# Kernel tuning notes

Measured on AMD Instinct MI355X. Metric: run time of the kernel, lower is better.

Reference implementation:

```python
import math
import numpy as np
import jax, jax.numpy as jnp

C = 8  # hidden multiplicity (num_channels)
B, N = 4, 4096

# ---------- real Wigner 3j (e3nn convention: Frobenius norm 1) ----------

def _su2_cg(l1, l2, l3):
    f = math.factorial
    def cg(m1, m2, m3):
        if m1 + m2 != m3:
            return 0.0
        pref = math.sqrt((2 * l3 + 1) * f(l3 + l1 - l2) * f(l3 - l1 + l2) * f(l1 + l2 - l3) / f(l1 + l2 + l3 + 1))
        pref *= math.sqrt(f(l3 + m3) * f(l3 - m3) * f(l1 - m1) * f(l1 + m1) * f(l2 - m2) * f(l2 + m2))
        s = 0.0
        for k in range(l1 + l2 - l3 + 1):
            d = [k, l1 + l2 - l3 - k, l1 - m1 - k, l2 + m2 - k, l3 - l2 + m1 + k, l3 - l1 - m2 + k]
            if min(d) < 0:
                continue
            s += (-1.0) ** k / np.prod([float(f(x)) for x in d])
        return pref * s
    out = np.zeros((2 * l1 + 1, 2 * l2 + 1, 2 * l3 + 1))
    for i, m1 in enumerate(range(-l1, l1 + 1)):
        for j, m2 in enumerate(range(-l2, l2 + 1)):
            for k, m3 in enumerate(range(-l3, l3 + 1)):
                out[i, j, k] = cg(m1, m2, m3)
    return out

def _q_real_to_complex(l):
    q = np.zeros((2 * l + 1, 2 * l + 1), dtype=np.complex128)
    rs2 = 1.0 / math.sqrt(2.0)
    for m in range(-l, 0):
        q[l + m, l + abs(m)] = rs2
        q[l + m, l - abs(m)] = -1j * rs2
    q[l, l] = 1.0
    for m in range(1, l + 1):
        q[l + m, l + abs(m)] = (-1) ** m * rs2
        q[l + m, l - abs(m)] = 1j * (-1) ** m * rs2
    return (-1j) ** l * q

def _w3j(l1, l2, l3):
    Q1, Q2, Q3 = _q_real_to_complex(l1), _q_real_to_complex(l2), _q_real_to_complex(l3)
    Cc = _su2_cg(l1, l2, l3).astype(np.complex128)
    Cr = np.real(np.einsum('ij,kl,mn,ikm->jln', Q1, Q2, np.conj(Q3), Cc))
    return (Cr / np.linalg.norm(Cr)).astype(np.float32)

# tensor-product paths (selection rules for 4e/6e inputs, 0e/2e SH, 4e/6e outputs)
VAL_PATHS = [(4, 0, 4), (4, 2, 4), (6, 2, 4), (4, 2, 6), (6, 0, 6), (6, 2, 6)]
OUT_PATHS = [(4, 4, 4), (4, 6, 4), (6, 4, 4), (6, 6, 4), (4, 4, 6), (4, 6, 6), (6, 4, 6), (6, 6, 6)]
# path normalization ('element'): fan-in = 3*C for tp_val outputs, 4*C^2 for tp_out outputs
W3J_VAL = [jnp.asarray(_w3j(*p) * math.sqrt((2 * p[2] + 1) / (3.0 * C))) for p in VAL_PATHS]
W3J_OUT = [jnp.asarray(_w3j(*p) * math.sqrt((2 * p[2] + 1) / (4.0 * C * C))) for p in OUT_PATHS]


def _forward(feat, sh_lr, log_s, pos_w, pos_b, w_lin_in, w_val, w_out, w_lin_out):
    b, n, _ = feat.shape
    f4, f6 = feat[..., :9], feat[..., 9:]                      # 1x4e, 1x6e
    f4n = f4 / jnp.maximum(jnp.linalg.norm(f4, axis=-1, keepdims=True), 1e-12)
    f6n = f6 / jnp.maximum(jnp.linalg.norm(f6, axis=-1, keepdims=True), 1e-12)
    s4, s6 = jnp.exp(log_s[0]), jnp.exp(log_s[1])
    scores = s4 * jnp.einsum('bnd,bmd->bnm', f4n, f4n) + s6 * jnp.einsum('bnd,bmd->bnm', f6n, f6n)
    pb = sh_lr @ pos_w + pos_b                                 # (N,)
    scores = scores + (pb[:, None] + pb[None, :])[None]
    attn = jax.nn.softmax(scores.astype(jnp.float32), axis=-1).astype(feat.dtype)

    h4 = f4[:, :, None, :] * w_lin_in[0][None, None, :, None]  # (B,N,C,9)
    h6 = f6[:, :, None, :] * w_lin_in[1][None, None, :, None]  # (B,N,C,13)

    y = {0: sh_lr[:, :1], 2: sh_lr[:, 1:]}                     # (N,1), (N,5)
    hx = {4: h4, 6: h6}
    v = {4: jnp.zeros((b, n, C, 9), feat.dtype), 6: jnp.zeros((b, n, C, 13), feat.dtype)}
    for p, (l1, l2, l3) in enumerate(VAL_PATHS):
        v[l3] = v[l3] + jnp.einsum('bnui,nj,ijk,uw->bnwk', hx[l1], y[l2], W3J_VAL[p], w_val[p])
    vals = jnp.concatenate([v[4].reshape(b, n, 9 * C), v[6].reshape(b, n, 13 * C)], axis=-1)

    ctx = jnp.einsum('bnm,bmd->bnd', attn, vals)               # (B,N,22C)
    cx = {4: ctx[..., :9 * C].reshape(b, n, C, 9), 6: ctx[..., 9 * C:].reshape(b, n, C, 13)}
    o = {4: jnp.zeros((b, n, C, 9), feat.dtype), 6: jnp.zeros((b, n, C, 13), feat.dtype)}
    for p, (l1, l2, l3) in enumerate(OUT_PATHS):
        o[l3] = o[l3] + jnp.einsum('bnui,bnvj,ijk,uvw->bnwk', hx[l1], cx[l2], W3J_OUT[p], w_out[p])

    inv_sc = 1.0 / math.sqrt(C)                                # lin_out fan_in = C
    d4 = jnp.einsum('bnui,u->bni', o[4], w_lin_out[0]) * inv_sc
    d6 = jnp.einsum('bnui,u->bni', o[6], w_lin_out[1]) * inv_sc
    return jnp.concatenate([d4, d6], axis=-1)                  # (B,N,22)


def setup_inputs() -> dict:
    key = jax.random.key(0)
    ks = jax.random.split(key, 8)
    feat = jax.random.normal(ks[0], (B, N, 22), jnp.float32)
    sh_lr = jax.random.normal(ks[1], (N, 6), jnp.float32)
    log_s = jnp.array([math.log(1.0 / 3.0), math.log(1.0 / math.sqrt(13.0))], jnp.float32)
    pos_w = 0.01 * jax.random.normal(ks[2], (6,), jnp.float32)
    pos_b = jnp.zeros((), jnp.float32)
    w_lin_in = jax.random.normal(ks[3], (2, C), jnp.float32)
    w_val = jax.random.normal(ks[4], (6, C, C), jnp.float32)
    w_out = jax.random.normal(ks[5], (8, C, C, C), jnp.float32)
    w_lin_out = jax.random.normal(ks[6], (2, C), jnp.float32)
    return dict(feat=feat, sh_lr=sh_lr, log_s=log_s, pos_w=pos_w, pos_b=pos_b,
                w_lin_in=w_lin_in, w_val=w_val, w_out=w_out, w_lin_out=w_lin_out)


def reference(feat, sh_lr, log_s, pos_w, pos_b, w_lin_in, w_val, w_out, w_lin_out):
    return _forward(feat, sh_lr, log_s, pos_w, pos_b, w_lin_in, w_val, w_out, w_lin_out)
```

## Files before the change

kernel.cpp:

```cpp
#include <hip/hip_runtime.h>
#include <cmath>

#define NN 4096
#define BB 4
#define CCH 8

#define OFF_W3JVAL 0
#define OFF_W3JOUT 2688
#define OFF_CTX0   13568
#define CTXS       1572864
#define OFFB_KGH   25220096ULL
#define OFFB_KGL   26268672ULL
#define OFFB_VG    27317248ULL
#define OFFB_WBH   30462976ULL
#define OFFB_WBL   30493696ULL

typedef short s16x8 __attribute__((ext_vector_type(8)));
typedef _Float16 f16x8 __attribute__((ext_vector_type(8)));
typedef float f32x4 __attribute__((ext_vector_type(4)));
typedef unsigned int u32x4 __attribute__((ext_vector_type(4)));
typedef unsigned int u32x2 __attribute__((ext_vector_type(2)));

static __device__ __forceinline__ unsigned short f2bf(float x){
  unsigned u = __float_as_uint(x);
  return (unsigned short)((u + 0x7FFFu + ((u >> 16) & 1u)) >> 16);
}
static __device__ __forceinline__ float bf2f(unsigned short h){
  return __uint_as_float(((unsigned)h) << 16);
}
static __device__ __forceinline__ unsigned pk2r(float v){
  unsigned short h = f2bf(v);
  unsigned short l = f2bf(v - bf2f(h));
  return ((unsigned)l << 16) | (unsigned)h;
}
static __device__ __forceinline__ unsigned short f2h(float x){
  return __builtin_bit_cast(unsigned short, (_Float16)x);
}
static __device__ __forceinline__ void unpk(u32x4 a, u32x4 b, s16x8& h, s16x8& l){
  u32x4 hw = { __builtin_amdgcn_perm(a[1],a[0],0x05040100u),
               __builtin_amdgcn_perm(a[3],a[2],0x05040100u),
               __builtin_amdgcn_perm(b[1],b[0],0x05040100u),
               __builtin_amdgcn_perm(b[3],b[2],0x05040100u)};
  u32x4 lw = { __builtin_amdgcn_perm(a[1],a[0],0x07060302u),
               __builtin_amdgcn_perm(a[3],a[2],0x07060302u),
               __builtin_amdgcn_perm(b[1],b[0],0x07060302u),
               __builtin_amdgcn_perm(b[3],b[2],0x07060302u)};
  h = __builtin_bit_cast(s16x8, hw);
  l = __builtin_bit_cast(s16x8, lw);
}

static __device__ __forceinline__ void qentf(int l, int r, int c, float& re, float& im){
  re=0.f; im=0.f;
  float s = ((l&3)==2)? -1.f : 1.f;
  const float rs2 = 0.70710678118654752440f;
  if(r < l){
    if(c == 2*l - r) re = s*rs2;
    else if(c == r)  im = -s*rs2;
  } else if(r == l){
    if(c == l) re = s;
  } else {
    float sg = ((r-l)&1)? -1.f : 1.f;
    if(c == r) re = s*sg*rs2;
    else if(c == 2*l - r) im = s*sg*rs2;
  }
}
__global__ __launch_bounds__(512) void k_tab(float* __restrict__ Wv, float* __restrict__ Wo){
  __shared__ float Ccf[2197];
  __shared__ float red[512];
  __shared__ double factS[20];
  int t = threadIdx.x;
  int p = blockIdx.x;
  if(t==0){
    double f=1.0; factS[0]=1.0;
    for(int i=1;i<20;i++){ f*=(double)i; factS[i]=f; }
  }
  const int L1[14]={4,4,6,4,6,6, 4,4,6,6,4,4,6,6};
  const int L2[14]={0,2,2,2,0,2, 4,6,4,6,4,6,4,6};
  const int L3[14]={4,4,4,6,6,6, 4,4,4,4,6,6,6,6};
  const int OFF[14]={0,81,486,1071,1656,1825, 0,729,1782,2835,4356,5409,6930,8451};
  int l1=L1[p], l2=L2[p], l3=L3[p];
  int d1=2*l1+1, d2=2*l2+1, d3=2*l3+1;
  int tot = d1*d2*d3;
  float* dst = (p<6) ? (Wv+OFF[p]) : (Wo+OFF[p]);
  float scale = (p<6) ? sqrtf((2.f*l3+1.f)/24.f) : sqrtf((2.f*l3+1.f)/256.f);
  __syncthreads();
  #pragma unroll 1
  for(int e=t; e<tot; e+=512){
    int i = e/(d2*d3), rem = e - i*(d2*d3), j = rem/d3, k = rem - j*d3;
    int m1=i-l1, m2=j-l2, m3=k-l3;
    double v=0.0;
    if(m1+m2==m3){
      double pref = sqrt((2.0*l3+1.0)*factS[l3+l1-l2]*factS[l3-l1+l2]*factS[l1+l2-l3]/factS[l1+l2+l3+1]);
      pref *= sqrt(factS[l3+m3]*factS[l3-m3]*factS[l1-m1]*factS[l1+m1]*factS[l2-m2]*factS[l2+m2]);
      double s=0.0;
      #pragma unroll 1
      for(int kk=0; kk<=l1+l2-l3; kk++){
        int dd0=kk, dd1=l1+l2-l3-kk, dd2=l1-m1-kk, dd3=l2+m2-kk, dd4=l3-l2+m1+kk, dd5=l3-l1-m2+kk;
        int mn=dd0;
        if(dd1<mn)mn=dd1; if(dd2<mn)mn=dd2; if(dd3<mn)mn=dd3; if(dd4<mn)mn=dd4; if(dd5<mn)mn=dd5;
        if(mn<0) continue;
        double prod = factS[dd0]*factS[dd1]*factS[dd2]*factS[dd3]*factS[dd4]*factS[dd5];
        s += ((kk&1)? -1.0:1.0)/prod;
      }
      v = pref*s;
    }
    Ccf[e]=(float)v;
  }
  __syncthreads();
  float nacc=0.f;
  #pragma unroll 1
  for(int e=t; e<tot; e+=512){
    int j = e/(d2*d3), rem = e - j*(d2*d3), l = rem/d3, n = rem - l*d3;
    float re = 0.f;
    #pragma unroll
    for(int ii=0; ii<2; ii++){
      int i = ii ? (2*l1 - j) : j;
      float q1r,q1i; qentf(l1,i,j,q1r,q1i);
      if(ii && i==j){ q1r=0.f; q1i=0.f; }
      #pragma unroll
      for(int kk=0; kk<2; kk++){
        int k = kk ? (2*l2 - l) : l;
        float q2r,q2i; qentf(l2,k,l,q2r,q2i);
        if(kk && k==l){ q2r=0.f; q2i=0.f; }
        float ar = q1r*q2r - q1i*q2i;
        float ai = q1r*q2i + q1i*q2r;
        #pragma unroll
        for(int mm=0; mm<2; mm++){
          int m = mm ? (2*l3 - n) : n;
          float q3r,q3i; qentf(l3,m,n,q3r,q3i);
          if(mm && m==n){ q3r=0.f; q3i=0.f; }
          float coef = ar*q3r + ai*q3i;
          re = fmaf(coef, Ccf[(i*d2+k)*d3+m], re);
        }
      }
    }
    dst[e]=re;
    nacc = fmaf(re,re,nacc);
  }
  red[t]=nacc;
  __syncthreads();
  #pragma unroll 1
  for(int s=256;s>0;s>>=1){
    if(t<s) red[t]+=red[t+s];
    __syncthreads();
  }
  float c = scale/sqrtf(red[0]);
  #pragma unroll 1
  for(int e=t; e<tot; e+=512) dst[e]*=c;
}

__global__ void k_weights(const float* __restrict__ wli, const float* __restrict__ wval,
                          const float* __restrict__ wout, const float* __restrict__ wlo,
                          const float* __restrict__ Wv,
                          unsigned short* __restrict__ WBH, unsigned short* __restrict__ WBL){
  __shared__ float bws[48];
  __shared__ float scs[64];
  __shared__ float As[24];
  int t = threadIdx.x;
  if(t<48){
    const int val_l1[6]={0,0,1,0,1,1};
    int p=t>>3, w=t&7;
    float s=0.f;
    for(int u=0;u<8;u++) s = fmaf(wli[val_l1[p]*8+u], wval[(p*8+u)*8+w], s);
    bws[t]=s;
  }
  {
    const int out_l1[8]={0,0,1,1,0,0,1,1};
    const int out_l3[8]={0,0,0,0,1,1,1,1};
    int p=t>>3, v=t&7;
    float s=0.f;
    for(int u=0;u<8;u++){
      float a=wli[out_l1[p]*8+u];
      for(int w=0;w<8;w++) s = fmaf(wout[((p*8+u)*8+v)*8+w]*a, wlo[out_l3[p]*8+w], s);
    }
    scs[t]=s*0.35355339059327373f;
  }
  __syncthreads();
  if(t<24){
    int p=t/3, i3=t-3*p;
    int vp = (p&1)*3 + i3;
    float s=0.f;
    for(int w=0;w<8;w++) s = fmaf(scs[p*8+w], bws[vp*8+w], s);
    As[t]=s;
  }
  __syncthreads();
  int base = blockIdx.x*960;
  for(int k=0;k<15;k++){
    int cell = base + k*64 + t;
    int f = cell/160, c = cell - f*160;
    float v = 0.f;
    if(f < 88 && c < 132){
      int seg = f/22, off = f - seg*22;
      int even = (off < 9);
      int p = 2*seg + (even?0:1);
      int jo = even ? off : off-9;
      int l1, i, jj;
      if(c < 54){ l1=4; i=c/6; jj=c-6*i; }
      else { int cc=c-54; l1=6; i=cc/6; jj=cc-6*i; }
      if(even){
        if(l1==4 && jj==0)      v = As[p*3+0]*Wv[i*9+jo];
        else if(l1==4)          v = As[p*3+1]*Wv[81+(i*5+jj-1)*9+jo];
        else if(jj>=1)          v = As[p*3+2]*Wv[486+(i*5+jj-1)*9+jo];
      } else {
        if(l1==4 && jj>=1)      v = As[p*3+0]*Wv[1071+(i*5+jj-1)*13+jo];
        else if(l1==6 && jj==0) v = As[p*3+1]*Wv[1656+i*13+jo];
        else if(l1==6)          v = As[p*3+2]*Wv[1825+(i*5+jj-1)*13+jo];
      }
    } else if(f==88 && c==132){
      v = 1.0f;
    }
    unsigned short h = f2bf(v);
    WBH[cell] = h;
    WBL[cell] = f2bf(v - bf2f(h));
  }
}

__launch_bounds__(128)
__global__ void k_prep(const float* __restrict__ feat, const float* __restrict__ sh,
                       const float* __restrict__ log_s, const float* __restrict__ pos_w,
                       const float* __restrict__ pos_b,
                       const unsigned short* __restrict__ WBH,
                       const unsigned short* __restrict__ WBL,
                       unsigned short* __restrict__ Kgh, unsigned short* __restrict__ Kgl,
                       unsigned short* __restrict__ Vg){
  __shared__ __align__(16) unsigned int Pbuf[16*164];
  __shared__ unsigned int Po[96*17];
  __shared__ float epbs[16];
  int tid = threadIdx.x;
  int w2 = tid >> 6, lane = tid & 63;
  int lm = lane & 15, quad = lane >> 4;
  int seg = w2*4 + quad;
  int panel = blockIdx.x >> 2, mt = blockIdx.x & 3;
  int idxp = panel*64 + mt*16 + lm;
  int n = idxp & (NN-1);
  const float* fp = feat + (size_t)idxp*22;
  const float* shp = sh + n*6;
  float f[22];
  #pragma unroll
  for(int c=0;c<22;c++) f[c]=fp[c];
  float y[6];
  #pragma unroll
  for(int j=0;j<6;j++) y[j]=shp[j];
  if(tid<16){
    float pb = pos_b[0];
    #pragma unroll
    for(int j=0;j<6;j++) pb = fmaf(y[j], pos_w[j], pb);
    epbs[lm] = __expf(pb);
    float n4=0.f, n6=0.f;
    #pragma unroll
    for(int c=0;c<9;c++) n4 += f[c]*f[c];
    #pragma unroll
    for(int c=9;c<22;c++) n6 += f[c]*f[c];
    n4 = fmaxf(sqrtf(n4), 1e-12f);
    n6 = fmaxf(sqrtf(n6), 1e-12f);
    float s4 = __expf(log_s[0]), s6 = __expf(log_s[1]);
    float a4 = sqrtf(s4)/n4, a6 = sqrtf(s6)/n6;
    unsigned short* kph = Kgh + (size_t)idxp*32;
    unsigned short* kpl = Kgl + (size_t)idxp*32;
    #pragma unroll
    for(int c=0;c<22;c++){
      float qv = f[c] * (c<9 ? a4 : a6);
      unsigned short h = f2bf(qv);
      kph[c]=h; kpl[c]=f2bf(qv - bf2f(h));
    }
    #pragma unroll
    for(int c=22;c<32;c++){ kph[c]=0; kpl[c]=0; }
  }
  #pragma unroll
  for(int j4=0;j4<5;j4++){
    u32x4 wv;
    #pragma unroll
    for(int e=0;e<4;e++){
      int c = seg*20 + j4*4 + e;
      float pv;
      if(c<54){ int i=c/6, jj=c-6*i; pv = f[i]*y[jj]; }
      else if(c<132){ int cc=c-54; int i=cc/6, jj=cc-6*i; pv = f[9+i]*y[jj]; }
      else if(c==132) pv = 1.0f;
      else pv = 0.0f;
      wv[e] = pk2r(pv);
    }
    *(u32x4*)&Pbuf[lm*164 + seg*20 + j4*4] = wv;
  }
  __syncthreads();
  f32x4 acc[3];
  #pragma unroll
  for(int ft=0;ft<3;ft++)
    #pragma unroll
    for(int i=0;i<4;i++) acc[ft][i]=0.f;
  for(int kc=0;kc<5;kc++){
    const u32x4* ap = (const u32x4*)&Pbuf[lm*164 + kc*32 + quad*8];
    s16x8 Ah, Al;
    unpk(ap[0], ap[1], Ah, Al);
    #pragma unroll
    for(int ft=0;ft<3;ft++){
      int ftg = w2*3 + ft;
      size_t bo = (size_t)(ftg*16+lm)*160 + kc*32 + quad*8;
      s16x8 Bh = *(const s16x8*)(WBH + bo);
      s16x8 Bl = *(const s16x8*)(WBL + bo);
      f32x4 a = acc[ft];
      a = __builtin_amdgcn_mfma_f32_16x16x32_bf16(Al, Bl, a, 0,0,0);
      a = __builtin_amdgcn_mfma_f32_16x16x32_bf16(Al, Bh, a, 0,0,0);
      a = __builtin_amdgcn_mfma_f32_16x16x32_bf16(Ah, Bl, a, 0,0,0);
      a = __builtin_amdgcn_mfma_f32_16x16x32_bf16(Ah, Bh, a, 0,0,0);
      acc[ft] = a;
    }
  }
  #pragma unroll
  for(int r=0;r<4;r++){
    float e = epbs[quad*4 + r];
    #pragma unroll
    for(int ft=0;ft<3;ft++){
      int ftg = w2*3 + ft;
      Po[(ftg*16+lm)*17 + quad*4 + r] = (unsigned)f2h(acc[ft][r]*e);
    }
  }
  __syncthreads();
  unsigned int* vO32 = (unsigned int*)(Vg + (size_t)panel*96*64);
  #pragma unroll
  for(int wv=0; wv<6; wv++){
    int idx2 = wv*128 + tid;
    int g = idx2 >> 3, j = idx2 & 7;
    unsigned lo = Po[g*17 + 2*j] & 0xFFFFu;
    unsigned hi = Po[g*17 + 2*j + 1] & 0xFFFFu;
    vO32[g*32 + mt*8 + j] = lo | (hi<<16);
  }
}

#define LDSK  0
#define LDSKL 4096
#define LDSV  8192
#define BUFB  20480
__global__ __launch_bounds__(512)
__attribute__((amdgpu_waves_per_eu(2, 2)))
void k_attn(const unsigned short* __restrict__ Kgh,
            const unsigned short* __restrict__ Kgl,
            const unsigned short* __restrict__ Vg,
            float* __restrict__ ctx0){
  __shared__ __align__(16) unsigned char lds[2*BUFB];
  int tid = threadIdx.x;
  int lane = tid & 63, w = tid >> 6;
  int lm = lane & 15, quad = lane >> 4;
  int blk = blockIdx.x;
  int b = blk & 3, kh = (blk>>2)&3, qb = blk >> 4;
  const unsigned short* KhB = Kgh + (size_t)b*NN*32;
  const unsigned short* KlB = Kgl + (size_t)b*NN*32;
  const unsigned short* VB  = Vg  + (size_t)b*64*96*64;
  float* ctx = ctx0 + (size_t)kh*CTXS + (size_t)b*NN*96;

  s16x8 qh[2], ql[2];
  #pragma unroll
  for(int q2=0;q2<2;q2++){
    size_t ro = (size_t)(qb*256 + w*32 + q2*16 + lm)*32 + (size_t)quad*8;
    qh[q2] = *(const s16x8*)(KhB + ro);
    ql[q2] = *(const s16x8*)(KlB + ro);
  }

  int kro = lm*64 + ((quad ^ ((lm>>1)&3))<<4);
  int vr0 = lm*128 + (((0*4+quad) ^ (lm&7))<<4);
  int vr1 = lm*128 + (((1*4+quad) ^ (lm&7))<<4);

  int dofs[3], sofs[3], sreg[3];
  #pragma unroll
  for(int rep=0;rep<3;rep++){
    int g = tid + 512*rep;
    if(g < 512){
      int gk = g & 255;
      int row = gk>>2, col = gk&3;
      int t = row>>4, rr = row&15;
      int kact = 32*(t&1) + 8*(rr>>2) + 4*(t>>1) + (rr&3);
      sreg[rep] = (g<256)? 0 : 1;
      sofs[rep] = kact*64 + col*16;
      dofs[rep] = ((g<256)? LDSK : LDSKL) + row*64 + ((col ^ ((row>>1)&3))<<4);
    }
    else if(g < 1280){ int gv=g-512; sreg[rep]=2; sofs[rep]=gv*16;
      dofs[rep] = LDSV + (gv>>3)*128 + (((gv&7) ^ ((gv>>3)&7))<<4); }
    else { sreg[rep]=-1; sofs[rep]=0; dofs[rep]=0; }
  }

  f32x4 acc[2][6];
  #pragma unroll
  for(int q2=0;q2<2;q2++)
    #pragma unroll
    for(int ft=0;ft<6;ft++)
      #pragma unroll
      for(int i=0;i<4;i++) acc[q2][ft][i]=0.f;

  u32x4 stg0, stg1, stg2;

#define MFB(A,Bv,C) __builtin_amdgcn_mfma_f32_16x16x32_bf16(A,Bv,C,0,0,0)
#define MFH(A,Bv,C) __builtin_amdgcn_mfma_f32_16x16x32_f16(A,Bv,C,0,0,0)

#define STG_ISSUE(T) { \
  const char* kb_ = (const char*)(KhB + (size_t)(kh*16+(T))*2048); \
  const char* lb_ = (const char*)(KlB + (size_t)(kh*16+(T))*2048); \
  const char* vb_ = (const char*)(VB  + (size_t)(kh*16+(T))*6144); \
  { const char* sp_ = (sreg[0]==0)? kb_ : (sreg[0]==1)? lb_ : vb_; \
    stg0 = *(const u32x4*)(sp_ + sofs[0]); } \
  { const char* sp_ = (sreg[1]==0)? kb_ : (sreg[1]==1)? lb_ : vb_; \
    stg1 = *(const u32x4*)(sp_ + sofs[1]); } \
  if(sreg[2]>=0){ stg2 = *(const u32x4*)(vb_ + sofs[2]); } }

#define STG_WRITE(BN) { \
  *(u32x4*)&lds[(BN)*BUFB + dofs[0]] = stg0; \
  *(u32x4*)&lds[(BN)*BUFB + dofs[1]] = stg1; \
  if(sreg[2]>=0){ *(u32x4*)&lds[(BN)*BUFB + dofs[2]] = stg2; } }

#define COMPUTE(B) { \
  unsigned Wt[2][4][2]; \
  _Pragma("unroll") \
  for(int kt=0;kt<4;kt++){ \
    s16x8 kfh = *(const s16x8*)&lds[(B)*BUFB + LDSK  + kt*1024 + kro]; \
    s16x8 kfl = *(const s16x8*)&lds[(B)*BUFB + LDSKL + kt*1024 + kro]; \
    _Pragma("unroll") \
    for(int q2=0;q2<2;q2++){ \
      f32x4 s_ = {0.f,0.f,0.f,0.f}; \
      s_ = MFB(kfl, qh[q2], s_); \
      s_ = MFB(kfh, ql[q2], s_); \
      s_ = MFB(kfh, qh[q2], s_); \
      Wt[q2][kt][0] = (unsigned)f2h(__expf(s_[0])) | ((unsigned)f2h(__expf(s_[1]))<<16); \
      Wt[q2][kt][1] = (unsigned)f2h(__expf(s_[2])) | ((unsigned)f2h(__expf(s_[3]))<<16); \
    } \
  } \
  _Pragma("unroll") \
  for(int c=0;c<2;c++){ \
    u32x4 paw0 = {Wt[0][c][0], Wt[0][c][1], Wt[0][c+2][0], Wt[0][c+2][1]}; \
    u32x4 paw1 = {Wt[1][c][0], Wt[1][c][1], Wt[1][c+2][0], Wt[1][c+2][1]}; \
    f16x8 PA0 = __builtin_bit_cast(f16x8, paw0); \
    f16x8 PA1 = __builtin_bit_cast(f16x8, paw1); \
    int vro_ = c ? vr1 : vr0; \
    _Pragma("unroll") \
    for(int ft=0;ft<6;ft++){ \
      f16x8 vf = *(const f16x8*)&lds[(B)*BUFB + LDSV + ft*2048 + vro_]; \
      acc[0][ft] = MFH(PA0, vf, acc[0][ft]); \
      acc[1][ft] = MFH(PA1, vf, acc[1][ft]); } \
  } }

  STG_ISSUE(0);
  STG_WRITE(0);
  __syncthreads();

  #pragma unroll 1
  for(int tp=0; tp<8; tp++){
    int t0 = 2*tp;
    STG_ISSUE(t0+1);
    COMPUTE(0);
    STG_WRITE(1);
    __syncthreads();
    if(t0+2 < 16){ STG_ISSUE(t0+2); }
    COMPUTE(1);
    if(t0+2 < 16){ STG_WRITE(0); }
    __syncthreads();
  }

#undef MFB
#undef MFH
#undef STG_ISSUE
#undef STG_WRITE
#undef COMPUTE

  #pragma unroll
  for(int q2=0;q2<2;q2++){
    #pragma unroll
    for(int ft=0;ft<6;ft++){
      int col = ft*16 + lm;
      #pragma unroll
      for(int r=0;r<4;r++){
        int row = qb*256 + w*32 + q2*16 + quad*4 + r;
        ctx[(size_t)row*96 + col] = acc[q2][ft][r];
      }
    }
  }
}

__launch_bounds__(256, 4)
__global__ void k_out(const float* __restrict__ feat, const float* __restrict__ ctxA,
                      const float* __restrict__ w3jout, float* __restrict__ out){
  __shared__ float gbuf[16*45];
  __shared__ float fbuf[16*24];
  __shared__ float dls[4*64*13];
  __shared__ float inv[16];
  int tid = threadIdx.x;
  int typ = blockIdx.x & 1;
  int n0 = (blockIdx.x>>1)*16;
  int gc0 = typ*44;
  for(int i=tid;i<16*44;i+=256){
    int pt=i/44, c=i-pt*44;
    const float* base = ctxA + (size_t)(n0+pt)*96 + gc0 + c;
    gbuf[pt*45+c] = base[0]+base[CTXS]+base[2*CTXS]+base[3*CTXS];
  }
  for(int i=tid;i<16*22;i+=256){
    int pt=i/22, c=i-pt*22;
    fbuf[pt*24+c] = feat[(size_t)(n0+pt)*22+c];
  }
  if(tid<16){
    const float* bd = ctxA + (size_t)(n0+tid)*96 + 88;
    inv[tid] = 1.0f/(bd[0]+bd[CTXS]+bd[2*CTXS]+bd[3*CTXS]);
  }
  __syncthreads();
  int lane = tid&63, w = tid>>6;
  int pt = lane&15, sub = lane>>4;
  float fR[13], gR[13], d[13];
  {
    int FB = (w&2)?9:0;
    int fn = (w&2)?13:9;
    #pragma unroll 13
    for(int i=0;i<13;i++) fR[i] = (i<fn) ? fbuf[pt*24 + FB + i] : 0.f;
    int GBl = (w==0)?0:(w==1)?9:(w==2)?22:31;
    int jn = (w&1)?13:9;
    #pragma unroll 13
    for(int j=0;j<13;j++) gR[j] = (j<jn) ? gbuf[pt*45 + GBl + j] : 0.f;
  }
  #pragma unroll 13
  for(int k=0;k<13;k++) d[k]=0.f;

#define PATHR(ID,JD,KD,WO) \
  _Pragma("unroll") \
  for(int ii=0;ii<((ID)+3)/4;ii++){ int i=sub+4*ii; if(i<(ID)){ float fv=fR[i]; \
    _Pragma("unroll") \
    for(int j=0;j<(JD);j++){ float val=fv*gR[j]; \
      const float* wp = w3jout + (WO) + (i*(JD)+j)*(KD); \
      _Pragma("unroll") \
      for(int k=0;k<(KD);k++) d[k] = fmaf(val, wp[k], d[k]); } } }

  int pcase = typ*4 + w;
  switch(pcase){
    case 0: PATHR(9,9,9, 0)       break;
    case 1: PATHR(9,13,9, 729)    break;
    case 2: PATHR(13,9,9, 1782)   break;
    case 3: PATHR(13,13,9, 2835)  break;
    case 4: PATHR(9,9,13, 4356)   break;
    case 5: PATHR(9,13,13, 5409)  break;
    case 6: PATHR(13,9,13, 6930)  break;
    default:PATHR(13,13,13, 8451) break;
  }
#undef PATHR
  {
    float* dp = &dls[(w*64+lane)*13];
    #pragma unroll 13
    for(int k=0;k<13;k++) dp[k]=d[k];
  }
  __syncthreads();
  {
    int KD = typ?13:9;
    int kb = typ?9:0;
    int pt2 = tid&15, kc = tid>>4;
    if(kc < KD){
      float s = 0.f;
      #pragma unroll
      for(int ww=0;ww<4;ww++)
        #pragma unroll
        for(int ss=0;ss<4;ss++)
          s += dls[(ww*64 + ss*16 + pt2)*13 + kc];
      out[(size_t)(n0+pt2)*22 + kb + kc] = s*inv[pt2];
    }
  }
}

extern "C" void kernel_launch(void* const* d_in, const int* in_sizes, int n_in,
                              void* d_out, int out_size, void* d_ws, size_t ws_size,
                              hipStream_t stream){
  (void)in_sizes; (void)n_in; (void)out_size; (void)ws_size;
  const float* feat =(const float*)d_in[0];
  const float* sh   =(const float*)d_in[1];
  const float* log_s=(const float*)d_in[2];
  const float* pos_w=(const float*)d_in[3];
  const float* pos_b=(const float*)d_in[4];
  const float* wli  =(const float*)d_in[5];
  const float* wval =(const float*)d_in[6];
  const float* wout =(const float*)d_in[7];
  const float* wlo  =(const float*)d_in[8];
  float* outp=(float*)d_out;
  float* wsf=(float*)d_ws;

  unsigned short* Kgh=(unsigned short*)((char*)d_ws + OFFB_KGH);
  unsigned short* Kgl=(unsigned short*)((char*)d_ws + OFFB_KGL);
  unsigned short* Vg =(unsigned short*)((char*)d_ws + OFFB_VG);
  unsigned short* WBH=(unsigned short*)((char*)d_ws + OFFB_WBH);
  unsigned short* WBL=(unsigned short*)((char*)d_ws + OFFB_WBL);

  hipLaunchKernelGGL(k_tab, dim3(14), dim3(512), 0, stream,
                     wsf+OFF_W3JVAL, wsf+OFF_W3JOUT);
  hipLaunchKernelGGL(k_weights, dim3(16), dim3(64), 0, stream,
                     wli, wval, wout, wlo, wsf+OFF_W3JVAL, WBH, WBL);
  hipLaunchKernelGGL(k_prep, dim3(1024), dim3(128), 0, stream,
                     feat, sh, log_s, pos_w, pos_b, WBH, WBL,
                     Kgh, Kgl, Vg);
  hipLaunchKernelGGL(k_attn, dim3(256), dim3(512), 0, stream,
                     Kgh, Kgl, Vg, wsf+OFF_CTX0);
  hipLaunchKernelGGL(k_out, dim3(2048), dim3(256), 0, stream,
                     feat, wsf+OFF_CTX0, wsf+OFF_W3JOUT, outp);
}
```

Measured before the change: 176.8 us.

## Software-pipeline attention: overlap next tile's scores/exp with current tile's PV MFMAs

Splits the per-tile attention compute into a score/exp stage (SPH) and a P·V stage (PVH). The P·V for one key tile now runs alongside the score MFMAs and exp for the next tile, using a three-buffer LDS ring and register-held exp weights. The goal is to hide the dependency chain from score MFMA to exp to f16 pack to PV MFMA, and to give the scheduler independent MFMA and VALU work to interleave. The cost is 1.5x LDS use and extra live registers for the buffered weights, which could cause spills under the fixed 2-waves-per-EU bound.

```diff
diff --git a/kernel.cpp b/kernel.cpp
--- a/kernel.cpp
+++ b/kernel.cpp
@@ -336,7 +336,7 @@
             const unsigned short* __restrict__ Kgl,
             const unsigned short* __restrict__ Vg,
             float* __restrict__ ctx0){
-  __shared__ __align__(16) unsigned char lds[2*BUFB];
+  __shared__ __align__(16) unsigned char lds[3*BUFB];
   int tid = threadIdx.x;
   int lane = tid & 63, w = tid >> 6;
   int lm = lane & 15, quad = lane >> 4;
@@ -385,6 +385,7 @@
       #pragma unroll
       for(int i=0;i<4;i++) acc[q2][ft][i]=0.f;
 
+  unsigned Wt[3][2][4][2];
   u32x4 stg0, stg1, stg2;
 
 #define MFB(A,Bv,C) __builtin_amdgcn_mfma_f32_16x16x32_bf16(A,Bv,C,0,0,0)
@@ -405,8 +406,7 @@
   *(u32x4*)&lds[(BN)*BUFB + dofs[1]] = stg1; \
   if(sreg[2]>=0){ *(u32x4*)&lds[(BN)*BUFB + dofs[2]] = stg2; } }
 
-#define COMPUTE(B) { \
-  unsigned Wt[2][4][2]; \
+#define SPH(B,WB) { \
   _Pragma("unroll") \
   for(int kt=0;kt<4;kt++){ \
     s16x8 kfh = *(const s16x8*)&lds[(B)*BUFB + LDSK  + kt*1024 + kro]; \
@@ -417,14 +417,16 @@
       s_ = MFB(kfl, qh[q2], s_); \
       s_ = MFB(kfh, ql[q2], s_); \
       s_ = MFB(kfh, qh[q2], s_); \
-      Wt[q2][kt][0] = (unsigned)f2h(__expf(s_[0])) | ((unsigned)f2h(__expf(s_[1]))<<16); \
-      Wt[q2][kt][1] = (unsigned)f2h(__expf(s_[2])) | ((unsigned)f2h(__expf(s_[3]))<<16); \
+      Wt[WB][q2][kt][0] = (unsigned)f2h(__expf(s_[0])) | ((unsigned)f2h(__expf(s_[1]))<<16); \
+      Wt[WB][q2][kt][1] = (unsigned)f2h(__expf(s_[2])) | ((unsigned)f2h(__expf(s_[3]))<<16); \
     } \
-  } \
+  } }
+
+#define PVH(B,WB) { \
   _Pragma("unroll") \
   for(int c=0;c<2;c++){ \
-    u32x4 paw0 = {Wt[0][c][0], Wt[0][c][1], Wt[0][c+2][0], Wt[0][c+2][1]}; \
-    u32x4 paw1 = {Wt[1][c][0], Wt[1][c][1], Wt[1][c+2][0], Wt[1][c+2][1]}; \
+    u32x4 paw0 = {Wt[WB][0][c][0], Wt[WB][0][c][1], Wt[WB][0][c+2][0], Wt[WB][0][c+2][1]}; \
+    u32x4 paw1 = {Wt[WB][1][c][0], Wt[WB][1][c][1], Wt[WB][1][c+2][0], Wt[WB][1][c+2][1]}; \
     f16x8 PA0 = __builtin_bit_cast(f16x8, paw0); \
     f16x8 PA1 = __builtin_bit_cast(f16x8, paw1); \
     int vro_ = c ? vr1 : vr0; \
@@ -438,25 +440,38 @@
   STG_ISSUE(0);
   STG_WRITE(0);
   __syncthreads();
+  STG_ISSUE(1);
+  SPH(0,0);
+  STG_WRITE(1);
+  __syncthreads();
 
   #pragma unroll 1
-  for(int tp=0; tp<8; tp++){
-    int t0 = 2*tp;
-    STG_ISSUE(t0+1);
-    COMPUTE(0);
-    STG_WRITE(1);
+  for(int it=0; it<5; it++){
+    int tA = 3*it + 1;
+    STG_ISSUE(tA+1);
+    SPH(1,1);
+    PVH(0,0);
+    STG_WRITE(2);
     __syncthreads();
-    if(t0+2 < 16){ STG_ISSUE(t0+2); }
-    COMPUTE(1);
-    if(t0+2 < 16){ STG_WRITE(0); }
+    STG_ISSUE(tA+2);
+    SPH(2,2);
+    PVH(1,1);
+    STG_WRITE(0);
     __syncthreads();
-  }
+    if(it<4){ STG_ISSUE(tA+3); }
+    SPH(0,0);
+    PVH(2,2);
+    if(it<4){ STG_WRITE(1); }
+    __syncthreads();
+  }
+  PVH(0,0);
 
 #undef MFB
 #undef MFH
 #undef STG_ISSUE
 #undef STG_WRITE
-#undef COMPUTE
+#undef SPH
+#undef PVH
 
   #pragma unroll
   for(int q2=0;q2<2;q2++){
```

After: 176.6 us. No clear change (-0.1%).

## Load V fragments directly from global into registers, bypassing LDS staging

Applied to the files above, without the earlier changes.

The attention kernel no longer stages V tiles through shared memory. Each wave now loads its own V MFMA fragments straight from global memory into registers per tile, and only the K high and low tiles stay double-buffered in LDS. This shrinks the LDS footprint and removes the V LDS writes and reads, at the cost of redundant global/L2 loads of V across the 8 waves and exposed load latency, since V is loaded right before use. The feat and sh loads in the prep kernel are also vectorized to float2.

```diff
diff --git a/kernel.cpp b/kernel.cpp
--- a/kernel.cpp
+++ b/kernel.cpp
@@ -237,10 +237,16 @@
   const float* shp = sh + n*6;
   float f[22];
   #pragma unroll
-  for(int c=0;c<22;c++) f[c]=fp[c];
+  for(int c=0;c<11;c++){
+    float2 v = *(const float2*)(fp + 2*c);
+    f[2*c] = v.x; f[2*c+1] = v.y;
+  }
   float y[6];
   #pragma unroll
-  for(int j=0;j<6;j++) y[j]=shp[j];
+  for(int j=0;j<3;j++){
+    float2 v = *(const float2*)(shp + 2*j);
+    y[2*j] = v.x; y[2*j+1] = v.y;
+  }
   if(tid<16){
     float pb = pos_b[0];
     #pragma unroll
@@ -328,15 +334,14 @@
 
 #define LDSK  0
 #define LDSKL 4096
-#define LDSV  8192
-#define BUFB  20480
+#define KBUF  8192
 __global__ __launch_bounds__(512)
 __attribute__((amdgpu_waves_per_eu(2, 2)))
 void k_attn(const unsigned short* __restrict__ Kgh,
             const unsigned short* __restrict__ Kgl,
             const unsigned short* __restrict__ Vg,
             float* __restrict__ ctx0){
-  __shared__ __align__(16) unsigned char lds[2*BUFB];
+  __shared__ __align__(16) unsigned char lds[2*KBUF];
   int tid = threadIdx.x;
   int lane = tid & 63, w = tid >> 6;
   int lm = lane & 15, quad = lane >> 4;
@@ -356,25 +361,17 @@
   }
 
   int kro = lm*64 + ((quad ^ ((lm>>1)&3))<<4);
-  int vr0 = lm*128 + (((0*4+quad) ^ (lm&7))<<4);
-  int vr1 = lm*128 + (((1*4+quad) ^ (lm&7))<<4);
-
-  int dofs[3], sofs[3], sreg[3];
-  #pragma unroll
-  for(int rep=0;rep<3;rep++){
-    int g = tid + 512*rep;
-    if(g < 512){
-      int gk = g & 255;
-      int row = gk>>2, col = gk&3;
-      int t = row>>4, rr = row&15;
-      int kact = 32*(t&1) + 8*(rr>>2) + 4*(t>>1) + (rr&3);
-      sreg[rep] = (g<256)? 0 : 1;
-      sofs[rep] = kact*64 + col*16;
-      dofs[rep] = ((g<256)? LDSK : LDSKL) + row*64 + ((col ^ ((row>>1)&3))<<4);
-    }
-    else if(g < 1280){ int gv=g-512; sreg[rep]=2; sofs[rep]=gv*16;
-      dofs[rep] = LDSV + (gv>>3)*128 + (((gv&7) ^ ((gv>>3)&7))<<4); }
-    else { sreg[rep]=-1; sofs[rep]=0; dofs[rep]=0; }
+  int vbase = lm*128 + quad*16;
+
+  int dofs, sofs; bool isH;
+  {
+    int g2 = tid & 255;
+    int row = g2>>2, col = g2&3;
+    int t = row>>4, rr = row&15;
+    int kact = 32*(t&1) + 8*(rr>>2) + 4*(t>>1) + (rr&3);
+    isH = (tid < 256);
+    sofs = kact*64 + col*16;
+    dofs = (isH ? LDSK : LDSKL) + row*64 + ((col ^ ((row>>1)&3))<<4);
   }
 
   f32x4 acc[2][6];
@@ -383,34 +380,34 @@
     #pragma unroll
     for(int ft=0;ft<6;ft++)
       #pragma unroll
-      for(int i=0;i<4;i++) acc[q2][ft][i]=0.f;
-
-  u32x4 stg0, stg1, stg2;
+      for(int i=0;i<4;i++) acc[2==2?q2:0][ft][i]=0.f;
+
+  unsigned Wt[2][4][2];
+  f16x8 vv[2][6];
+  u32x4 stg0;
 
 #define MFB(A,Bv,C) __builtin_amdgcn_mfma_f32_16x16x32_bf16(A,Bv,C,0,0,0)
 #define MFH(A,Bv,C) __builtin_amdgcn_mfma_f32_16x16x32_f16(A,Bv,C,0,0,0)
 
 #define STG_ISSUE(T) { \
-  const char* kb_ = (const char*)(KhB + (size_t)(kh*16+(T))*2048); \
-  const char* lb_ = (const char*)(KlB + (size_t)(kh*16+(T))*2048); \
-  const char* vb_ = (const char*)(VB  + (size_t)(kh*16+(T))*6144); \
-  { const char* sp_ = (sreg[0]==0)? kb_ : (sreg[0]==1)? lb_ : vb_; \
-    stg0 = *(const u32x4*)(sp_ + sofs[0]); } \
-  { const char* sp_ = (sreg[1]==0)? kb_ : (sreg[1]==1)? lb_ : vb_; \
-    stg1 = *(const u32x4*)(sp_ + sofs[1]); } \
-  if(sreg[2]>=0){ stg2 = *(const u32x4*)(vb_ + sofs[2]); } }
-
-#define STG_WRITE(BN) { \
-  *(u32x4*)&lds[(BN)*BUFB + dofs[0]] = stg0; \
-  *(u32x4*)&lds[(BN)*BUFB + dofs[1]] = stg1; \
-  if(sreg[2]>=0){ *(u32x4*)&lds[(BN)*BUFB + dofs[2]] = stg2; } }
-
-#define COMPUTE(B) { \
-  unsigned Wt[2][4][2]; \
+  const unsigned short* kp_ = (isH ? KhB : KlB) + (size_t)(kh*16+(T))*2048; \
+  stg0 = *(const u32x4*)((const char*)kp_ + sofs); }
+
+#define STG_WRITE(BN) { *(u32x4*)&lds[(BN)*KBUF + dofs] = stg0; }
+
+#define VLOAD(T) { \
+  const char* vb_ = (const char*)(VB + (size_t)(kh*16+(T))*6144) + vbase; \
+  _Pragma("unroll") \
+  for(int c=0;c<2;c++) \
+  _Pragma("unroll") \
+  for(int ft=0;ft<6;ft++) \
+    vv[c][ft] = *(const f16x8*)(vb_ + ft*2048 + c*64); }
+
+#define SPH(B) { \
   _Pragma("unroll") \
   for(int kt=0;kt<4;kt++){ \
-    s16x8 kfh = *(const s16x8*)&lds[(B)*BUFB + LDSK  + kt*1024 + kro]; \
-    s16x8 kfl = *(const s16x8*)&lds[(B)*BUFB + LDSKL + kt*1024 + kro]; \
+    s16x8 kfh = *(const s16x8*)&lds[(B)*KBUF + LDSK  + kt*1024 + kro]; \
+    s16x8 kfl = *(const s16x8*)&lds[(B)*KBUF + LDSKL + kt*1024 + kro]; \
     _Pragma("unroll") \
     for(int q2=0;q2<2;q2++){ \
       f32x4 s_ = {0.f,0.f,0.f,0.f}; \
@@ -420,19 +417,19 @@
       Wt[q2][kt][0] = (unsigned)f2h(__expf(s_[0])) | ((unsigned)f2h(__expf(s_[1]))<<16); \
       Wt[q2][kt][1] = (unsigned)f2h(__expf(s_[2])) | ((unsigned)f2h(__expf(s_[3]))<<16); \
     } \
-  } \
+  } }
+
+#define PVH() { \
   _Pragma("unroll") \
   for(int c=0;c<2;c++){ \
     u32x4 paw0 = {Wt[0][c][0], Wt[0][c][1], Wt[0][c+2][0], Wt[0][c+2][1]}; \
     u32x4 paw1 = {Wt[1][c][0], Wt[1][c][1], Wt[1][c+2][0], Wt[1][c+2][1]}; \
     f16x8 PA0 = __builtin_bit_cast(f16x8, paw0); \
     f16x8 PA1 = __builtin_bit_cast(f16x8, paw1); \
-    int vro_ = c ? vr1 : vr0; \
     _Pragma("unroll") \
     for(int ft=0;ft<6;ft++){ \
-      f16x8 vf = *(const f16x8*)&lds[(B)*BUFB + LDSV + ft*2048 + vro_]; \
-      acc[0][ft] = MFH(PA0, vf, acc[0][ft]); \
-      acc[1][ft] = MFH(PA1, vf, acc[1][ft]); } \
+      acc[0][ft] = MFH(PA0, vv[c][ft], acc[0][ft]); \
+      acc[1][ft] = MFH(PA1, vv[c][ft], acc[1][ft]); } \
   } }
 
   STG_ISSUE(0);
@@ -443,11 +440,15 @@
   for(int tp=0; tp<8; tp++){
     int t0 = 2*tp;
     STG_ISSUE(t0+1);
-    COMPUTE(0);
+    VLOAD(t0);
+    SPH(0);
+    PVH();
     STG_WRITE(1);
     __syncthreads();
     if(t0+2 < 16){ STG_ISSUE(t0+2); }
-    COMPUTE(1);
+    VLOAD(t0+1);
+    SPH(1);
+    PVH();
     if(t0+2 < 16){ STG_WRITE(0); }
     __syncthreads();
   }
@@ -456,7 +457,9 @@
 #undef MFH
 #undef STG_ISSUE
 #undef STG_WRITE
-#undef COMPUTE
+#undef VLOAD
+#undef SPH
+#undef PVH
 
   #pragma unroll
   for(int q2=0;q2<2;q2++){
```

Result: slower. 202.6 us (+14.6%).
